# Kernel tuning notes

Measured on AMD Instinct MI355X. Metric: run time of the kernel, lower is better.

The kernel has to match this reference:

```python
import jax, jax.numpy as jnp
import numpy as np

D_MODEL = 1024
NUM_HEADS = 16
DEPTH = D_MODEL // NUM_HEADS


def setup_inputs() -> dict:
    key = jax.random.key(0)
    ks = jax.random.split(key, 9)
    B, S = 2, 2048
    scale = 1.0 / np.sqrt(D_MODEL)
    inputs = jax.random.normal(ks[0], (B, S, D_MODEL), dtype=jnp.float32)
    wq = jax.random.normal(ks[1], (D_MODEL, D_MODEL), dtype=jnp.float32) * scale
    wk = jax.random.normal(ks[2], (D_MODEL, D_MODEL), dtype=jnp.float32) * scale
    wv = jax.random.normal(ks[3], (D_MODEL, D_MODEL), dtype=jnp.float32) * scale
    wo = jax.random.normal(ks[4], (D_MODEL, D_MODEL), dtype=jnp.float32) * scale
    bq = jnp.zeros((D_MODEL,), jnp.float32)
    bk = jnp.zeros((D_MODEL,), jnp.float32)
    bv = jnp.zeros((D_MODEL,), jnp.float32)
    bo = jnp.zeros((D_MODEL,), jnp.float32)
    return {"inputs": inputs, "wq": wq, "bq": bq, "wk": wk, "bk": bk,
            "wv": wv, "bv": bv, "wo": wo, "bo": bo}


def _split_heads(x):
    # [B, S, D] -> [B, H, S, depth]
    B, S, _ = x.shape
    return x.reshape(B, S, NUM_HEADS, DEPTH).transpose(0, 2, 1, 3)


def reference(inputs, wq, bq, wk, bk, wv, bv, wo, bo):
    B, S, _ = inputs.shape
    q = _split_heads(inputs @ wq + bq)   # [B,H,S,d]
    k = _split_heads(inputs @ wk + bk)
    v = _split_heads(inputs @ wv + bv)
    scale = 1.0 / jnp.sqrt(jnp.float32(DEPTH))
    logits = jnp.einsum('bhqd,bhkd->bhqk', q, k) * scale  # [B,H,S,S]
    attn = jax.nn.softmax(logits, axis=-1)
    # dropout is identity at inference time
    out = jnp.einsum('bhqk,bhkd->bhqd', attn, v)          # [B,H,S,d]
    out = out.transpose(0, 2, 1, 3).reshape(B, S, D_MODEL)
    return out @ wo + bo
```

## Files before the change

### kernel.cpp

```cpp
#include <hip/hip_runtime.h>
#include <cstdint>
#include <cstddef>

#define D_MODEL 1024
#define S_LEN   2048
#define NHEAD   16
#define DHEAD   64
#define BSZ     2
#define LOG2E   1.44269504088896f

typedef short  short8   __attribute__((ext_vector_type(8)));
typedef float  floatx4  __attribute__((ext_vector_type(4)));
typedef float  floatx16 __attribute__((ext_vector_type(16)));
typedef unsigned short u16x4 __attribute__((ext_vector_type(4)));

__device__ inline unsigned short f2b(float f) {
  union { float f; unsigned int u; } v; v.f = f;
  unsigned int r = v.u + 0x7FFFu + ((v.u >> 16) & 1u);
  return (unsigned short)(r >> 16);
}

__device__ inline void gload_lds16(const void* g, void* l) {
  __builtin_amdgcn_global_load_lds(
      (const __attribute__((address_space(1))) unsigned int*)g,
      (__attribute__((address_space(3))) unsigned int*)l, 16, 0, 0);
}

__global__ __launch_bounds__(256) void k_prep(
    const float* __restrict__ x,
    const float* __restrict__ wq, const float* __restrict__ wk,
    const float* __restrict__ wv, const float* __restrict__ wo,
    unsigned short* __restrict__ xb, unsigned short* __restrict__ wqkvT,
    unsigned short* __restrict__ woT) {
  int bid = blockIdx.x;
  if (bid < 4096) {
    int i = bid * 256 + threadIdx.x;
    float4 f = ((const float4*)x)[i];
    u16x4 o;
    o[0] = f2b(f.x); o[1] = f2b(f.y); o[2] = f2b(f.z); o[3] = f2b(f.w);
    ((u16x4*)xb)[i] = o;
    return;
  }
  __shared__ float tile[32][33];
  int r = bid - 4096;
  int which = r >> 10, tl = r & 1023;
  const float* src = (which == 0) ? wq : (which == 1) ? wk : (which == 2) ? wv : wo;
  unsigned short* dst = (which < 3) ? (wqkvT + (size_t)which * 1024 * 1024) : woT;
  int bx = (tl & 31) * 32;
  int by = (tl >> 5) * 32;
  int tx = threadIdx.x & 31, ty0 = threadIdx.x >> 5;
  #pragma unroll
  for (int i = 0; i < 4; i++) {
    int ty = ty0 + i * 8;
    tile[ty][tx] = src[(size_t)(by + ty) * D_MODEL + bx + tx];
  }
  __syncthreads();
  #pragma unroll
  for (int i = 0; i < 4; i++) {
    int ty = ty0 + i * 8;
    dst[(size_t)(bx + ty) * D_MODEL + by + tx] = f2b(tile[tx][ty]);
  }
}

__device__ inline void gemm_tiles(const unsigned short* __restrict__ A,
                                  const unsigned short* __restrict__ Bt,
                                  int m0, int n0, short* As, short* Bs,
                                  floatx4 acc[4][4]) {
  const int t = threadIdx.x, w = t >> 6, lane = t & 63;
  const int wr = w >> 1, wc = w & 1, g = lane >> 4, l15 = lane & 15;
  floatx4 zf = {0.f, 0.f, 0.f, 0.f};
  #pragma unroll
  for (int m = 0; m < 4; m++)
    #pragma unroll
    for (int n = 0; n < 4; n++) acc[m][n] = zf;

  auto stage = [&](int kt, int b) {
    #pragma unroll
    for (int i = 0; i < 2; i++) {
      int p = i * 256 + t;
      int row = p >> 2, ce = (p & 3) << 3;
      gload_lds16(A  + (size_t)(m0 + row) * D_MODEL + kt * 32 + ce,
                  (char*)As + b * 8192 + i * 4096 + w * 1024);
      gload_lds16(Bt + (size_t)(n0 + row) * D_MODEL + kt * 32 + ce,
                  (char*)Bs + b * 8192 + i * 4096 + w * 1024);
    }
  };

  stage(0, 0);
  __syncthreads();
  #pragma unroll 2
  for (int kt = 0; kt < D_MODEL / 32; kt++) {
    int b = kt & 1;
    if (kt < D_MODEL / 32 - 1) stage(kt + 1, b ^ 1);

    short8 af[4], bfr[4];
    #pragma unroll
    for (int m = 0; m < 4; m++)
      af[m] = *(const short8*)((const char*)As + b * 8192 + (wr * 64 + m * 16 + l15) * 64 + g * 16);
    #pragma unroll
    for (int n = 0; n < 4; n++)
      bfr[n] = *(const short8*)((const char*)Bs + b * 8192 + (wc * 64 + n * 16 + l15) * 64 + g * 16);
    __builtin_amdgcn_s_setprio(1);
    #pragma unroll
    for (int m = 0; m < 4; m++)
      #pragma unroll
      for (int n = 0; n < 4; n++)
        acc[m][n] = __builtin_amdgcn_mfma_f32_16x16x32_bf16(af[m], bfr[n], acc[m][n], 0, 0, 0);
    __builtin_amdgcn_s_setprio(0);
    __syncthreads();
  }
}

__global__ __launch_bounds__(256) void k_gemm_qkv(
    const unsigned short* __restrict__ xb, const unsigned short* __restrict__ wT,
    const float* __restrict__ bq, const float* __restrict__ bk, const float* __restrict__ bv,
    unsigned short* __restrict__ qb, unsigned short* __restrict__ kb,
    unsigned short* __restrict__ vtb) {
  __shared__ __align__(16) short As[8192], Bs[8192];
  floatx4 acc[4][4];
  int m0 = blockIdx.y * 128, n0 = blockIdx.x * 128;
  gemm_tiles(xb, wT, m0, n0, As, Bs, acc);
  int t = threadIdx.x, w = t >> 6, lane = t & 63;
  int wr = w >> 1, wc = w & 1, g = lane >> 4, l15 = lane & 15;
  #pragma unroll
  for (int m = 0; m < 4; m++) {
    #pragma unroll
    for (int n = 0; n < 4; n++) {
      int row0 = m0 + wr * 64 + m * 16 + g * 4;
      int col  = n0 + wc * 64 + n * 16 + l15;
      int sel = col >> 10, c = col & 1023;
      int h = c >> 6, dd = c & 63;
      int b_ = row0 >> 11, ss = row0 & 2047;
      if (sel == 2) {
        u16x4 o;
        #pragma unroll
        for (int j = 0; j < 4; j++) o[j] = f2b(acc[m][n][j] + bv[c]);
        *(u16x4*)(vtb + ((size_t)(b_ * NHEAD + h) * DHEAD + dd) * S_LEN + ss) = o;
      } else {
        const float* bias = (sel == 0) ? bq : bk;
        unsigned short* dst = (sel == 0) ? qb : kb;
        float sc = (sel == 0) ? 0.125f * LOG2E : 1.0f;
        #pragma unroll
        for (int j = 0; j < 4; j++) {
          float v = (acc[m][n][j] + bias[c]) * sc;
          dst[(size_t)((b_ * NHEAD + h) * S_LEN + ss + j) * DHEAD + dd] = f2b(v);
        }
      }
    }
  }
}

__global__ __launch_bounds__(128) void k_attn(
    const unsigned short* __restrict__ Q, const unsigned short* __restrict__ K,
    const unsigned short* __restrict__ Vt, unsigned short* __restrict__ O) {
  __shared__ __align__(16) char lds[32768];
  char* KsB0 = lds;
  char* KsB1 = lds + 8192;
  char* VsB0 = lds + 16384;
  char* VsB1 = lds + 24576;

  int L = blockIdx.x;
  int bh = (L & 7) + 8 * ((L >> 3) >> 5);
  int qt = (L >> 3) & 31;

  int t = threadIdx.x, w = t >> 6, lane = t & 63, l31 = lane & 31, hi = lane >> 5;
  const unsigned short* Qh = Q + (size_t)bh * S_LEN * DHEAD;
  const unsigned short* Kh = K + (size_t)bh * S_LEN * DHEAD;
  const unsigned short* Vh = Vt + (size_t)bh * DHEAD * S_LEN;
  int q0 = qt * 64;

  #pragma unroll
  for (int i = 0; i < 4; i++) {
    int p = i * 128 + t;
    int row = p >> 3;
    int sb = ((p & 7) ^ ((row ^ (row >> 3)) & 7)) << 4;
    gload_lds16(Qh + (size_t)(q0 + row) * DHEAD + (sb >> 1), VsB1 + i * 2048 + w * 1024);
    gload_lds16(Kh + (size_t)row * DHEAD + (sb >> 1),        KsB0 + i * 2048 + w * 1024);
    gload_lds16(Vh + (size_t)row * S_LEN + (sb >> 1),        VsB0 + i * 2048 + w * 1024);
  }
  __syncthreads();

  const int fr0 = ((l31 ^ (l31 >> 3)) & 7) << 4;
  short8 qf[4];
  #pragma unroll
  for (int ds = 0; ds < 4; ds++)
    qf[ds] = *(const short8*)(VsB1 + (w * 32 + l31) * 128 + ((32 * ds + 16 * hi) ^ fr0 ^ (w << 6)));
  __asm__ volatile("s_waitcnt lgkmcnt(0)" ::: "memory");
  __syncthreads();

  floatx16 accd[2];
  #pragma unroll
  for (int dt = 0; dt < 2; dt++)
    #pragma unroll
    for (int r = 0; r < 16; r++) accd[dt][r] = 0.f;
  float lsum = 0.f;

  #pragma unroll 2
  for (int kt = 0; kt < S_LEN / 64; kt++) {
    int b = kt & 1;
    char* Ks = b ? KsB1 : KsB0;
    char* Vs = b ? VsB1 : VsB0;
    if (kt < S_LEN / 64 - 1) {
      char* Kn = b ? KsB0 : KsB1;
      char* Vn = b ? VsB0 : VsB1;
      #pragma unroll
      for (int i = 0; i < 4; i++) {
        int p = i * 128 + t;
        int row = p >> 3;
        int sb = ((p & 7) ^ ((row ^ (row >> 3)) & 7)) << 4;
        gload_lds16(Kh + (size_t)((kt + 1) * 64 + row) * DHEAD + (sb >> 1), Kn + i * 2048 + w * 1024);
        gload_lds16(Vh + (size_t)row * S_LEN + (kt + 1) * 64 + (sb >> 1),   Vn + i * 2048 + w * 1024);
      }
    }

    #pragma unroll
    for (int kvt = 0; kvt < 2; kvt++) {
      short8 kf[4];
      #pragma unroll
      for (int ds = 0; ds < 4; ds++)
        kf[ds] = *(const short8*)(Ks + (kvt * 32 + l31) * 128 + ((32 * ds + 16 * hi) ^ fr0 ^ (kvt << 6)));
      floatx16 s;
      #pragma unroll
      for (int r = 0; r < 16; r++) s[r] = 0.f;
      __builtin_amdgcn_s_setprio(1);
      #pragma unroll
      for (int ds = 0; ds < 4; ds++)
        s = __builtin_amdgcn_mfma_f32_32x32x16_bf16(kf[ds], qf[ds], s, 0, 0, 0);
      __builtin_amdgcn_s_setprio(0);

      float p[16];
      #pragma unroll
      for (int r = 0; r < 16; r++) { p[r] = __builtin_amdgcn_exp2f(s[r]); lsum += p[r]; }
      unsigned int pk0[4], pk1[4];
      #pragma unroll
      for (int m = 0; m < 4; m++) {
        __asm__("v_cvt_pk_bf16_f32 %0, %1, %2" : "=v"(pk0[m]) : "v"(p[4 * m + 0]), "v"(p[4 * m + 1]));
        __asm__("v_cvt_pk_bf16_f32 %0, %1, %2" : "=v"(pk1[m]) : "v"(p[4 * m + 2]), "v"(p[4 * m + 3]));
      }
      short8 pf[2];
      #pragma unroll
      for (int ks = 0; ks < 2; ks++) {
        unsigned int a0 = pk0[2 * ks], a1 = pk1[2 * ks];
        unsigned int b0 = pk0[2 * ks + 1], b1 = pk1[2 * ks + 1];
        __asm__("v_permlane32_swap_b32 %0, %1" : "+v"(a0), "+v"(b0));
        __asm__("v_permlane32_swap_b32 %0, %1" : "+v"(a1), "+v"(b1));
        union { unsigned int u[4]; short8 s8; } fu;
        fu.u[0] = a0; fu.u[1] = a1; fu.u[2] = b0; fu.u[3] = b1;
        pf[ks] = fu.s8;
      }

      __builtin_amdgcn_s_setprio(1);
      #pragma unroll
      for (int ks = 0; ks < 2; ks++) {
        int slice = kvt * 2 + ks;
        #pragma unroll
        for (int dt = 0; dt < 2; dt++) {
          short8 vf = *(const short8*)(Vs + (dt * 32 + l31) * 128 + ((32 * slice + 16 * hi) ^ fr0 ^ (dt << 6)));
          accd[dt] = __builtin_amdgcn_mfma_f32_32x32x16_bf16(vf, pf[ks], accd[dt], 0, 0, 0);
        }
      }
      __builtin_amdgcn_s_setprio(0);
    }
    __syncthreads();
  }

  float lfull = lsum + __shfl_xor(lsum, 32);
  float inv = 1.0f / lfull;
  int b_ = bh >> 4, h = bh & 15;
  int q = q0 + w * 32 + l31;
  unsigned short* Orow = O + (size_t)(b_ * S_LEN + q) * D_MODEL + h * 64;
  #pragma unroll
  for (int dt = 0; dt < 2; dt++) {
    #pragma unroll
    for (int r = 0; r < 16; r++) {
      int d = dt * 32 + (r & 3) + 8 * (r >> 2) + 4 * hi;
      Orow[d] = f2b(accd[dt][r] * inv);
    }
  }
}

__global__ __launch_bounds__(256) void k_gemm_out(
    const unsigned short* __restrict__ ab, const unsigned short* __restrict__ woT,
    const float* __restrict__ bo, float* __restrict__ out) {
  __shared__ __align__(16) short As[2][2048], Bs[2][4096];
  const int t = threadIdx.x, w = t >> 6, lane = t & 63;
  const int g = lane >> 4, l15 = lane & 15;
  int m0 = blockIdx.y * 64, n0 = blockIdx.x * 128;
  floatx4 acc[4][2];
  floatx4 zf = {0.f, 0.f, 0.f, 0.f};
  #pragma unroll
  for (int m = 0; m < 4; m++) { acc[m][0] = zf; acc[m][1] = zf; }

  auto stage = [&](int kt, int b) {
    {
      int row = t >> 2, ce = (t & 3) << 3;
      gload_lds16(ab + (size_t)(m0 + row) * D_MODEL + kt * 32 + ce,
                  (char*)As[b] + w * 1024);
    }
    #pragma unroll
    for (int i = 0; i < 2; i++) {
      int p = i * 256 + t;
      int row = p >> 2, ce = (p & 3) << 3;
      gload_lds16(woT + (size_t)(n0 + row) * D_MODEL + kt * 32 + ce,
                  (char*)Bs[b] + i * 4096 + w * 1024);
    }
  };

  stage(0, 0);
  __syncthreads();
  #pragma unroll 2
  for (int kt = 0; kt < D_MODEL / 32; kt++) {
    int b = kt & 1;
    if (kt < D_MODEL / 32 - 1) stage(kt + 1, b ^ 1);
    short8 af[4], bfr[2];
    #pragma unroll
    for (int m = 0; m < 4; m++)
      af[m] = *(const short8*)((const char*)As[b] + (m * 16 + l15) * 64 + g * 16);
    #pragma unroll
    for (int n = 0; n < 2; n++)
      bfr[n] = *(const short8*)((const char*)Bs[b] + (w * 32 + n * 16 + l15) * 64 + g * 16);
    __builtin_amdgcn_s_setprio(1);
    #pragma unroll
    for (int m = 0; m < 4; m++)
      #pragma unroll
      for (int n = 0; n < 2; n++)
        acc[m][n] = __builtin_amdgcn_mfma_f32_16x16x32_bf16(af[m], bfr[n], acc[m][n], 0, 0, 0);
    __builtin_amdgcn_s_setprio(0);
    __syncthreads();
  }

  #pragma unroll
  for (int m = 0; m < 4; m++) {
    #pragma unroll
    for (int n = 0; n < 2; n++) {
      #pragma unroll
      for (int j = 0; j < 4; j++) {
        int row = m0 + m * 16 + g * 4 + j;
        int col = n0 + w * 32 + n * 16 + l15;
        out[(size_t)row * D_MODEL + col] = acc[m][n][j] + bo[col];
      }
    }
  }
}

extern "C" void kernel_launch(void* const* d_in, const int* in_sizes, int n_in,
                              void* d_out, int out_size, void* d_ws, size_t ws_size,
                              hipStream_t stream) {
  const float* x  = (const float*)d_in[0];
  const float* wq = (const float*)d_in[1];
  const float* bq = (const float*)d_in[2];
  const float* wk = (const float*)d_in[3];
  const float* bk = (const float*)d_in[4];
  const float* wv = (const float*)d_in[5];
  const float* bv = (const float*)d_in[6];
  const float* wo = (const float*)d_in[7];
  const float* bo = (const float*)d_in[8];
  float* out = (float*)d_out;

  char* ws = (char*)d_ws;
  unsigned short* xb    = (unsigned short*)(ws);
  unsigned short* wqkvT = (unsigned short*)(ws + 8388608);
  unsigned short* woT   = (unsigned short*)(ws + 14680064);
  unsigned short* qb    = (unsigned short*)(ws + 16777216);
  unsigned short* kb    = (unsigned short*)(ws + 25165824);
  unsigned short* vtb   = (unsigned short*)(ws + 33554432);
  unsigned short* ab    = xb;

  k_prep<<<8192, 256, 0, stream>>>(x, wq, wk, wv, wo, xb, wqkvT, woT);
  k_gemm_qkv<<<dim3(24, 32), 256, 0, stream>>>(xb, wqkvT, bq, bk, bv, qb, kb, vtb);
  k_attn<<<1024, 128, 0, stream>>>(qb, kb, vtb, ab);
  k_gemm_out<<<dim3(8, 64), 256, 0, stream>>>(ab, woT, bo, out);
}
```

Baseline: 213.2 us.

## Triple-buffer GEMM loads with explicit vmcnt waits and deepen attention KV prefetch

Both GEMM kernels move from double to triple-buffered LDS staging, prefetching two k-tiles ahead. Each iteration uses a partial s_waitcnt vmcnt plus a single s_barrier in place of __syncthreads, so global loads stay in flight across iterations. The attention kernel prefetches KV two tiles ahead, issuing the next load after a trailing barrier, and writes its output with vectorized 4-element stores. LDS use per block rises and occupancy hints are added, and the hand-counted vmcnt values must match the number of outstanding loads exactly or correctness breaks.

New measurement: 195.3 us. -8.4%, faster.

```diff
diff --git a/kernel.cpp b/kernel.cpp
--- a/kernel.cpp
+++ b/kernel.cpp
@@ -13,6 +13,14 @@
 typedef float  floatx4  __attribute__((ext_vector_type(4)));
 typedef float  floatx16 __attribute__((ext_vector_type(16)));
 typedef unsigned short u16x4 __attribute__((ext_vector_type(4)));
+
+#define VM8  __asm__ volatile("s_waitcnt vmcnt(8)" ::: "memory")
+#define VM4  __asm__ volatile("s_waitcnt vmcnt(4)" ::: "memory")
+#define VM3  __asm__ volatile("s_waitcnt vmcnt(3)" ::: "memory")
+#define VM0  __asm__ volatile("s_waitcnt vmcnt(0)" ::: "memory")
+#define LG0  __asm__ volatile("s_waitcnt lgkmcnt(0)" ::: "memory")
+#define SBAR __builtin_amdgcn_s_barrier()
+#define SCHED __builtin_amdgcn_sched_barrier(0)
 
 __device__ inline unsigned short f2b(float f) {
   union { float f; unsigned int u; } v; v.f = f;
@@ -64,8 +72,7 @@
 
 __device__ inline void gemm_tiles(const unsigned short* __restrict__ A,
                                   const unsigned short* __restrict__ Bt,
-                                  int m0, int n0, short* As, short* Bs,
-                                  floatx4 acc[4][4]) {
+                                  int m0, int n0, char* lds, floatx4 acc[4][4]) {
   const int t = threadIdx.x, w = t >> 6, lane = t & 63;
   const int wr = w >> 1, wc = w & 1, g = lane >> 4, l15 = lane & 15;
   floatx4 zf = {0.f, 0.f, 0.f, 0.f};
@@ -74,32 +81,37 @@
     #pragma unroll
     for (int n = 0; n < 4; n++) acc[m][n] = zf;
 
-  auto stage = [&](int kt, int b) {
+  auto stage = [&](int kt, int bi) {
     #pragma unroll
     for (int i = 0; i < 2; i++) {
       int p = i * 256 + t;
       int row = p >> 2, ce = (p & 3) << 3;
       gload_lds16(A  + (size_t)(m0 + row) * D_MODEL + kt * 32 + ce,
-                  (char*)As + b * 8192 + i * 4096 + w * 1024);
+                  lds + bi * 8192 + i * 4096 + w * 1024);
       gload_lds16(Bt + (size_t)(n0 + row) * D_MODEL + kt * 32 + ce,
-                  (char*)Bs + b * 8192 + i * 4096 + w * 1024);
+                  lds + 24576 + bi * 8192 + i * 4096 + w * 1024);
     }
   };
 
   stage(0, 0);
-  __syncthreads();
-  #pragma unroll 2
-  for (int kt = 0; kt < D_MODEL / 32; kt++) {
-    int b = kt & 1;
-    if (kt < D_MODEL / 32 - 1) stage(kt + 1, b ^ 1);
-
+  stage(1, 1);
+  int bi = 0;
+  for (int kt = 0; kt < 32; kt++) {
+    if (kt < 31) { VM4; } else { VM0; }
+    SBAR; SCHED;
+    if (kt < 30) {
+      int b2 = bi + 2; if (b2 >= 3) b2 -= 3;
+      stage(kt + 2, b2);
+    }
+    const char* As = lds + bi * 8192;
+    const char* Bs = lds + 24576 + bi * 8192;
     short8 af[4], bfr[4];
     #pragma unroll
     for (int m = 0; m < 4; m++)
-      af[m] = *(const short8*)((const char*)As + b * 8192 + (wr * 64 + m * 16 + l15) * 64 + g * 16);
+      af[m] = *(const short8*)(As + (wr * 64 + m * 16 + l15) * 64 + g * 16);
     #pragma unroll
     for (int n = 0; n < 4; n++)
-      bfr[n] = *(const short8*)((const char*)Bs + b * 8192 + (wc * 64 + n * 16 + l15) * 64 + g * 16);
+      bfr[n] = *(const short8*)(Bs + (wc * 64 + n * 16 + l15) * 64 + g * 16);
     __builtin_amdgcn_s_setprio(1);
     #pragma unroll
     for (int m = 0; m < 4; m++)
@@ -107,19 +119,19 @@
       for (int n = 0; n < 4; n++)
         acc[m][n] = __builtin_amdgcn_mfma_f32_16x16x32_bf16(af[m], bfr[n], acc[m][n], 0, 0, 0);
     __builtin_amdgcn_s_setprio(0);
-    __syncthreads();
-  }
-}
-
-__global__ __launch_bounds__(256) void k_gemm_qkv(
+    bi++; if (bi == 3) bi = 0;
+  }
+}
+
+__global__ __launch_bounds__(256, 3) void k_gemm_qkv(
     const unsigned short* __restrict__ xb, const unsigned short* __restrict__ wT,
     const float* __restrict__ bq, const float* __restrict__ bk, const float* __restrict__ bv,
     unsigned short* __restrict__ qb, unsigned short* __restrict__ kb,
     unsigned short* __restrict__ vtb) {
-  __shared__ __align__(16) short As[8192], Bs[8192];
+  __shared__ __align__(16) char lds[49152];
   floatx4 acc[4][4];
   int m0 = blockIdx.y * 128, n0 = blockIdx.x * 128;
-  gemm_tiles(xb, wT, m0, n0, As, Bs, acc);
+  gemm_tiles(xb, wT, m0, n0, lds, acc);
   int t = threadIdx.x, w = t >> 6, lane = t & 63;
   int wr = w >> 1, wc = w & 1, g = lane >> 4, l15 = lane & 15;
   #pragma unroll
@@ -169,15 +181,27 @@
   const unsigned short* Vh = Vt + (size_t)bh * DHEAD * S_LEN;
   int q0 = qt * 64;
 
+  auto stageKV = [&](int kt, int b) {
+    char* Kd = b ? KsB1 : KsB0;
+    char* Vd = b ? VsB1 : VsB0;
+    #pragma unroll
+    for (int i = 0; i < 4; i++) {
+      int p = i * 128 + t;
+      int row = p >> 3;
+      int sb = ((p & 7) ^ ((row ^ (row >> 3)) & 7)) << 4;
+      gload_lds16(Kh + (size_t)(kt * 64 + row) * DHEAD + (sb >> 1), Kd + i * 2048 + w * 1024);
+      gload_lds16(Vh + (size_t)row * S_LEN + kt * 64 + (sb >> 1),   Vd + i * 2048 + w * 1024);
+    }
+  };
+
   #pragma unroll
   for (int i = 0; i < 4; i++) {
     int p = i * 128 + t;
     int row = p >> 3;
     int sb = ((p & 7) ^ ((row ^ (row >> 3)) & 7)) << 4;
     gload_lds16(Qh + (size_t)(q0 + row) * DHEAD + (sb >> 1), VsB1 + i * 2048 + w * 1024);
-    gload_lds16(Kh + (size_t)row * DHEAD + (sb >> 1),        KsB0 + i * 2048 + w * 1024);
-    gload_lds16(Vh + (size_t)row * S_LEN + (sb >> 1),        VsB0 + i * 2048 + w * 1024);
-  }
+  }
+  stageKV(0, 0);
   __syncthreads();
 
   const int fr0 = ((l31 ^ (l31 >> 3)) & 7) << 4;
@@ -185,8 +209,9 @@
   #pragma unroll
   for (int ds = 0; ds < 4; ds++)
     qf[ds] = *(const short8*)(VsB1 + (w * 32 + l31) * 128 + ((32 * ds + 16 * hi) ^ fr0 ^ (w << 6)));
-  __asm__ volatile("s_waitcnt lgkmcnt(0)" ::: "memory");
-  __syncthreads();
+  LG0;
+  SBAR; SCHED;
+  stageKV(1, 1);
 
   floatx16 accd[2];
   #pragma unroll
@@ -200,18 +225,8 @@
     int b = kt & 1;
     char* Ks = b ? KsB1 : KsB0;
     char* Vs = b ? VsB1 : VsB0;
-    if (kt < S_LEN / 64 - 1) {
-      char* Kn = b ? KsB0 : KsB1;
-      char* Vn = b ? VsB0 : VsB1;
-      #pragma unroll
-      for (int i = 0; i < 4; i++) {
-        int p = i * 128 + t;
-        int row = p >> 3;
-        int sb = ((p & 7) ^ ((row ^ (row >> 3)) & 7)) << 4;
-        gload_lds16(Kh + (size_t)((kt + 1) * 64 + row) * DHEAD + (sb >> 1), Kn + i * 2048 + w * 1024);
-        gload_lds16(Vh + (size_t)row * S_LEN + (kt + 1) * 64 + (sb >> 1),   Vn + i * 2048 + w * 1024);
-      }
-    }
+    if (kt < S_LEN / 64 - 1) { VM8; } else { VM0; }
+    SBAR; SCHED;
 
     #pragma unroll
     for (int kvt = 0; kvt < 2; kvt++) {
@@ -261,7 +276,9 @@
       }
       __builtin_amdgcn_s_setprio(0);
     }
-    __syncthreads();
+
+    SBAR; SCHED;
+    if (kt < S_LEN / 64 - 2) stageKV(kt + 2, b);
   }
 
   float lfull = lsum + __shfl_xor(lsum, 32);
@@ -272,17 +289,19 @@
   #pragma unroll
   for (int dt = 0; dt < 2; dt++) {
     #pragma unroll
-    for (int r = 0; r < 16; r++) {
-      int d = dt * 32 + (r & 3) + 8 * (r >> 2) + 4 * hi;
-      Orow[d] = f2b(accd[dt][r] * inv);
-    }
-  }
-}
-
-__global__ __launch_bounds__(256) void k_gemm_out(
+    for (int m = 0; m < 4; m++) {
+      u16x4 ov;
+      #pragma unroll
+      for (int j = 0; j < 4; j++) ov[j] = f2b(accd[dt][4 * m + j] * inv);
+      *(u16x4*)(Orow + dt * 32 + 8 * m + 4 * hi) = ov;
+    }
+  }
+}
+
+__global__ __launch_bounds__(256, 2) void k_gemm_out(
     const unsigned short* __restrict__ ab, const unsigned short* __restrict__ woT,
     const float* __restrict__ bo, float* __restrict__ out) {
-  __shared__ __align__(16) short As[2][2048], Bs[2][4096];
+  __shared__ __align__(16) char lds[36864];
   const int t = threadIdx.x, w = t >> 6, lane = t & 63;
   const int g = lane >> 4, l15 = lane & 15;
   int m0 = blockIdx.y * 64, n0 = blockIdx.x * 128;
@@ -291,34 +310,40 @@
   #pragma unroll
   for (int m = 0; m < 4; m++) { acc[m][0] = zf; acc[m][1] = zf; }
 
-  auto stage = [&](int kt, int b) {
+  auto stage = [&](int kt, int bi) {
     {
       int row = t >> 2, ce = (t & 3) << 3;
       gload_lds16(ab + (size_t)(m0 + row) * D_MODEL + kt * 32 + ce,
-                  (char*)As[b] + w * 1024);
+                  lds + bi * 4096 + w * 1024);
     }
     #pragma unroll
     for (int i = 0; i < 2; i++) {
       int p = i * 256 + t;
       int row = p >> 2, ce = (p & 3) << 3;
       gload_lds16(woT + (size_t)(n0 + row) * D_MODEL + kt * 32 + ce,
-                  (char*)Bs[b] + i * 4096 + w * 1024);
+                  lds + 12288 + bi * 8192 + i * 4096 + w * 1024);
     }
   };
 
   stage(0, 0);
-  __syncthreads();
-  #pragma unroll 2
-  for (int kt = 0; kt < D_MODEL / 32; kt++) {
-    int b = kt & 1;
-    if (kt < D_MODEL / 32 - 1) stage(kt + 1, b ^ 1);
+  stage(1, 1);
+  int bi = 0;
+  for (int kt = 0; kt < 32; kt++) {
+    if (kt < 31) { VM3; } else { VM0; }
+    SBAR; SCHED;
+    if (kt < 30) {
+      int b2 = bi + 2; if (b2 >= 3) b2 -= 3;
+      stage(kt + 2, b2);
+    }
+    const char* As = lds + bi * 4096;
+    const char* Bs = lds + 12288 + bi * 8192;
     short8 af[4], bfr[2];
     #pragma unroll
     for (int m = 0; m < 4; m++)
-      af[m] = *(const short8*)((const char*)As[b] + (m * 16 + l15) * 64 + g * 16);
+      af[m] = *(const short8*)(As + (m * 16 + l15) * 64 + g * 16);
     #pragma unroll
     for (int n = 0; n < 2; n++)
-      bfr[n] = *(const short8*)((const char*)Bs[b] + (w * 32 + n * 16 + l15) * 64 + g * 16);
+      bfr[n] = *(const short8*)(Bs + (w * 32 + n * 16 + l15) * 64 + g * 16);
     __builtin_amdgcn_s_setprio(1);
     #pragma unroll
     for (int m = 0; m < 4; m++)
@@ -326,7 +351,7 @@
       for (int n = 0; n < 2; n++)
         acc[m][n] = __builtin_amdgcn_mfma_f32_16x16x32_bf16(af[m], bfr[n], acc[m][n], 0, 0, 0);
     __builtin_amdgcn_s_setprio(0);
-    __syncthreads();
+    bi++; if (bi == 3) bi = 0;
   }
 
   #pragma unroll
```
